# Kernel tuning notes

Hardware: AMD Instinct MI355X
Metric: run time of the kernel (lower is better)

## Reference

```python
import jax, jax.numpy as jnp
import numpy as np

N_NODES = 50000
N_EDGES = 600000
BAG = 16
VOCAB = 10000
EMB = 128
HID = 128
N_CLASSES = 10
N_GRAPHS = 512
PAD_IDX = 1


def setup_inputs() -> dict:
    key = jax.random.key(0)
    ks = jax.random.split(key, 12)
    x_tokens = jax.random.randint(ks[0], (N_NODES, BAG), 0, VOCAB)
    src = jax.random.randint(ks[1], (N_EDGES,), 0, N_NODES)
    dst = jax.random.randint(ks[2], (N_EDGES,), 0, N_NODES)
    edge_index = jnp.stack([src, dst])
    batch = jnp.sort(jax.random.randint(ks[3], (N_NODES,), 0, N_GRAPHS))
    # rows 0,1 are zero in the original (weights[2:] filled from pretrained vectors)
    emb_table = (jax.random.normal(ks[4], (VOCAB, EMB)) * 0.02).at[:2].set(0.0)
    s = 1.0 / np.sqrt(EMB)
    w1_l = jax.random.normal(ks[5], (HID, EMB)) * s
    b1 = jnp.zeros((HID,), jnp.float32)
    w1_r = jax.random.normal(ks[6], (HID, EMB)) * s
    w2_l = jax.random.normal(ks[7], (HID, HID)) * s
    b2 = jnp.zeros((HID,), jnp.float32)
    w2_r = jax.random.normal(ks[8], (HID, HID)) * s
    w_out = jax.random.normal(ks[9], (N_CLASSES, HID)) * s
    b_out = jnp.zeros((N_CLASSES,), jnp.float32)
    return {"x_tokens": x_tokens, "edge_index": edge_index, "batch": batch,
            "emb_table": emb_table, "w1_l": w1_l, "b1": b1, "w1_r": w1_r,
            "w2_l": w2_l, "b2": b2, "w2_r": w2_r, "w_out": w_out, "b_out": b_out}


def _embedding_bag_mean(tokens, table):
    # nn.EmbeddingBag mode='mean' with padding_idx: padding tokens excluded from mean
    emb = table[tokens]                                  # [N, BAG, D]
    mask = (tokens != PAD_IDX)[..., None].astype(table.dtype)
    total = jnp.sum(emb * mask, axis=1)                  # [N, D]
    cnt = jnp.clip(jnp.sum(mask, axis=1), 1.0)           # [N, 1]
    return total / cnt


def _sage_conv(x, src, dst, w_l, b_l, w_r):
    # PyG SAGEConv: lin_l(mean_{j in N(i)} x_j) + lin_r(x_i); lin_r has no bias
    n = x.shape[0]
    msg_sum = jax.ops.segment_sum(x[src], dst, num_segments=n)           # [N, D]
    deg = jax.ops.segment_sum(jnp.ones((src.shape[0], 1), x.dtype), dst,
                              num_segments=n)                             # [N, 1]
    aggr = msg_sum / jnp.clip(deg, 1.0)
    return aggr @ w_l.T + b_l + x @ w_r.T


def reference(x_tokens, edge_index, batch, emb_table, w1_l, b1, w1_r,
              w2_l, b2, w2_r, w_out, b_out):
    src, dst = edge_index[0], edge_index[1]
    x = _embedding_bag_mean(x_tokens, emb_table)                 # [N, EMB]
    x = jax.nn.relu(_sage_conv(x, src, dst, w1_l, b1, w1_r))     # [N, HID]
    x = jax.nn.relu(_sage_conv(x, src, dst, w2_l, b2, w2_r))     # [N, HID]
    # global_mean_pool over graph ids
    g_sum = jax.ops.segment_sum(x, batch, num_segments=N_GRAPHS)
    g_cnt = jax.ops.segment_sum(jnp.ones((x.shape[0], 1), x.dtype), batch,
                                num_segments=N_GRAPHS)
    g = g_sum / jnp.clip(g_cnt, 1.0)                             # [G, HID]
    return g @ w_out.T + b_out                                   # [G, C]
```

## Files before the change

### kernel.cpp

```cpp
#include <hip/hip_runtime.h>
#include <hip/hip_bf16.h>

#define NN 50000
#define NE 600000
#define BAG 16
#define EMB 128
#define HID 128
#define NC 10
#define NG 512
#define PAD_IDX 1
#define VOCAB 10000
#define SLOTS 64
#define TPAIRS (VOCAB * EMB / 2)
#define WPAIRS (4 * HID * EMB / 2)
#define EMVB (NN / 16)
#define NTILES ((NN + 127) / 128)

typedef __attribute__((ext_vector_type(8))) short v8s;
typedef __attribute__((ext_vector_type(4))) float v4f;

__device__ __forceinline__ float bflo(unsigned u) { return __uint_as_float(u << 16); }
__device__ __forceinline__ float bfhi(unsigned u) { return __uint_as_float(u & 0xffff0000u); }
__device__ __forceinline__ unsigned short f2bf(float f) {
    unsigned u = __float_as_uint(f);
    return (unsigned short)((u + 0x7fffu + ((u >> 16) & 1u)) >> 16);
}
__device__ __forceinline__ void acc8(float* a, v8s v) {
    unsigned* u = (unsigned*)&v;
#pragma unroll
    for (int j = 0; j < 4; j++) {
        a[2 * j] += bflo(u[j]);
        a[2 * j + 1] += bfhi(u[j]);
    }
}

__global__ void k_conv(const float* __restrict__ t, unsigned short* __restrict__ tb,
                       const float* __restrict__ w1l, const float* __restrict__ w1r,
                       const float* __restrict__ w2l, const float* __restrict__ w2r,
                       unsigned short* __restrict__ wbf, int* __restrict__ cnt,
                       float* __restrict__ gsum, float* __restrict__ gcnt) {
    int i = blockIdx.x * blockDim.x + threadIdx.x;
    if (i < NN) cnt[i] = 0;
    if (i < NG * HID) gsum[i] = 0.f;
    if (i < NG) gcnt[i] = 0.f;
    if (i < TPAIRS) {
        float2 v = *(const float2*)(t + (size_t)i * 2);
        unsigned lo = f2bf(v.x), hi = f2bf(v.y);
        *(unsigned*)(tb + (size_t)i * 2) = lo | (hi << 16);
    } else if (i < TPAIRS + WPAIRS) {
        int j = i - TPAIRS;
        int k = j * 2;
        int arr = k >> 14;
        int o = k & 16383;
        const float* w = (arr == 0) ? w1l : (arr == 1) ? w1r : (arr == 2) ? w2l : w2r;
        float2 v = *(const float2*)(w + o);
        unsigned lo = f2bf(v.x), hi = f2bf(v.y);
        *(unsigned*)(wbf + k) = lo | (hi << 16);
    }
}

__global__ __launch_bounds__(256) void k_scatem(const int* __restrict__ src,
                                                const int* __restrict__ dst,
                                                int* __restrict__ cnt,
                                                int* __restrict__ slots,
                                                const int* __restrict__ tokens,
                                                const unsigned short* __restrict__ table,
                                                unsigned short* __restrict__ x0) {
    int b = blockIdx.x;
    int tid = threadIdx.x;

    int e = b * 256 + tid;
    int s_src = 0, s_dst = 0, p = SLOTS;
    bool has_e = (e < NE);
    if (has_e) {
        s_src = src[e];
        s_dst = dst[e];
        p = atomicAdd(&cnt[s_dst], 1);
    }

    int sl = tid & 15;
    int node = b * 16 + (tid >> 4);
    const int* tp = tokens + node * BAG;
    int tk[16];
    *(int4*)(tk) = *(const int4*)(tp);
    *(int4*)(tk + 4) = *(const int4*)(tp + 4);
    *(int4*)(tk + 8) = *(const int4*)(tp + 8);
    *(int4*)(tk + 12) = *(const int4*)(tp + 12);
    int c = 0;
#pragma unroll
    for (int t = 0; t < BAG; t++) c += (tk[t] != PAD_IDX);
    float a[8];
#pragma unroll
    for (int j = 0; j < 8; j++) a[j] = 0.f;
#pragma unroll
    for (int h = 0; h < 2; h++) {
        v8s v[8];
#pragma unroll
        for (int t = 0; t < 8; t++)
            v[t] = *(const v8s*)(table + (size_t)tk[h * 8 + t] * EMB + sl * 8);
#pragma unroll
        for (int t = 0; t < 8; t++) acc8(a, v[t]);
    }
    float inv = 1.0f / (float)(c > 0 ? c : 1);
    uint4 o;
    o.x = f2bf(a[0] * inv) | ((unsigned)f2bf(a[1] * inv) << 16);
    o.y = f2bf(a[2] * inv) | ((unsigned)f2bf(a[3] * inv) << 16);
    o.z = f2bf(a[4] * inv) | ((unsigned)f2bf(a[5] * inv) << 16);
    o.w = f2bf(a[6] * inv) | ((unsigned)f2bf(a[7] * inv) << 16);
    *(uint4*)(x0 + (size_t)node * EMB + sl * 8) = o;

    if (has_e && p < SLOTS) slots[(size_t)s_dst * SLOTS + p] = s_src;
}

__global__ __launch_bounds__(256) void k_aggr(const unsigned short* __restrict__ x,
                                              const int* __restrict__ cnt,
                                              const int* __restrict__ slots,
                                              unsigned short* __restrict__ aggr) {
    int node = blockIdx.x * 4 + (threadIdx.x >> 6);
    int lane = threadIdx.x & 63;
    if (node >= NN) return;
    int deg = cnt[node];
    int m = deg > SLOTS ? SLOTS : deg;
    int g = lane >> 4, sl = lane & 15;
    float a[8];
#pragma unroll
    for (int j = 0; j < 8; j++) a[j] = 0.f;
    int idx_l = slots[(size_t)node * SLOTS + ((lane < m) ? lane : 0)];
    int i = 0;
    for (; i + 8 <= m; i += 8) {
        int t0 = __shfl(idx_l, i + g, 64);
        int t1 = __shfl(idx_l, i + 4 + g, 64);
        v8s v0 = *(const v8s*)(x + (size_t)t0 * HID + sl * 8);
        v8s v1 = *(const v8s*)(x + (size_t)t1 * HID + sl * 8);
        acc8(a, v0);
        acc8(a, v1);
    }
    for (; i + 4 <= m; i += 4) {
        int t0 = __shfl(idx_l, i + g, 64);
        v8s v0 = *(const v8s*)(x + (size_t)t0 * HID + sl * 8);
        acc8(a, v0);
    }
    int rem = m - i;
    if (rem > 0) {
        int t0 = __shfl(idx_l, (g < rem) ? i + g : i, 64);
        v8s v0 = *(const v8s*)(x + (size_t)t0 * HID + sl * 8);
        if (g < rem) acc8(a, v0);
    }
#pragma unroll
    for (int j = 0; j < 8; j++) {
        a[j] += __shfl_xor(a[j], 16, 64);
        a[j] += __shfl_xor(a[j], 32, 64);
    }
    float inv = 1.0f / (float)(deg > 0 ? deg : 1);
    if (g == 0) {
        uint4 o;
        o.x = f2bf(a[0] * inv) | ((unsigned)f2bf(a[1] * inv) << 16);
        o.y = f2bf(a[2] * inv) | ((unsigned)f2bf(a[3] * inv) << 16);
        o.z = f2bf(a[4] * inv) | ((unsigned)f2bf(a[5] * inv) << 16);
        o.w = f2bf(a[6] * inv) | ((unsigned)f2bf(a[7] * inv) << 16);
        *(uint4*)(aggr + (size_t)node * HID + sl * 8) = o;
    }
}

__device__ __forceinline__ void sage_kloop(int row0, const unsigned short* __restrict__ xa,
                                           const unsigned short* __restrict__ xr,
                                           const unsigned short* __restrict__ wl,
                                           const unsigned short* __restrict__ wr,
                                           unsigned short* As, unsigned short* Bs,
                                           v4f acc[2][8]) {
    int tid = threadIdx.x;
    int wave = tid >> 6, lane = tid & 63;
    int q = lane >> 4, l16 = lane & 15;
    for (int kc = 0; kc < 8; kc++) {
        const unsigned short* Ag = (kc < 4) ? xa : xr;
        const unsigned short* Bg = (kc < 4) ? wl : wr;
        int koff = (kc & 3) * 32;
#pragma unroll
        for (int it = 0; it < 2; it++) {
            int seg = tid + it * 256;
            int r = seg >> 2, sg = seg & 3;
            int gr = row0 + r;
            if (gr > NN - 1) gr = NN - 1;
            v8s a = *(const v8s*)(Ag + (size_t)gr * HID + koff + sg * 8);
            *(v8s*)(As + r * 32 + sg * 8) = a;
            v8s b = *(const v8s*)(Bg + (size_t)r * HID + koff + sg * 8);
            *(v8s*)(Bs + r * 32 + sg * 8) = b;
        }
        __syncthreads();
        v8s a0 = *(const v8s*)(As + (wave * 32 + l16) * 32 + q * 8);
        v8s a1 = *(const v8s*)(As + (wave * 32 + 16 + l16) * 32 + q * 8);
#pragma unroll
        for (int nt = 0; nt < 8; nt++) {
            v8s b = *(const v8s*)(Bs + (nt * 16 + l16) * 32 + q * 8);
            acc[0][nt] = __builtin_amdgcn_mfma_f32_16x16x32_bf16(a0, b, acc[0][nt], 0, 0, 0);
            acc[1][nt] = __builtin_amdgcn_mfma_f32_16x16x32_bf16(a1, b, acc[1][nt], 0, 0, 0);
        }
        __syncthreads();
    }
}

__global__ __launch_bounds__(256) void k_sage(const unsigned short* __restrict__ xa,
                                              const unsigned short* __restrict__ xr,
                                              const unsigned short* __restrict__ wl,
                                              const unsigned short* __restrict__ wr,
                                              const float* __restrict__ bias,
                                              unsigned short* __restrict__ out) {
    __shared__ unsigned short As[128 * 32];
    __shared__ unsigned short Bs[128 * 32];
    int row0 = blockIdx.x * 128;
    v4f acc[2][8];
#pragma unroll
    for (int m = 0; m < 2; m++)
#pragma unroll
        for (int n = 0; n < 8; n++) acc[m][n] = (v4f){0.f, 0.f, 0.f, 0.f};
    sage_kloop(row0, xa, xr, wl, wr, As, Bs, acc);
    int tid = threadIdx.x;
    int wave = tid >> 6, lane = tid & 63;
    int q = lane >> 4, l16 = lane & 15;
#pragma unroll
    for (int nt = 0; nt < 8; nt++) {
        int col = nt * 16 + l16;
        float bv = bias[col];
#pragma unroll
        for (int mt = 0; mt < 2; mt++) {
#pragma unroll
            for (int r = 0; r < 4; r++) {
                int row = row0 + wave * 32 + mt * 16 + q * 4 + r;
                if (row < NN) {
                    float v = acc[mt][nt][r] + bv;
                    v = v > 0.f ? v : 0.f;
                    out[(size_t)row * HID + col] = f2bf(v);
                }
            }
        }
    }
}

__global__ __launch_bounds__(256) void k_sagepool(const unsigned short* __restrict__ xa,
                                                  const unsigned short* __restrict__ xr,
                                                  const unsigned short* __restrict__ wl,
                                                  const unsigned short* __restrict__ wr,
                                                  const float* __restrict__ bias,
                                                  const int* __restrict__ batch,
                                                  float* __restrict__ gsum,
                                                  float* __restrict__ gcnt) {
    __shared__ unsigned short smem[128 * 128];
    unsigned short* As = smem;
    unsigned short* Bs = smem + 128 * 32;
    int row0 = blockIdx.x * 128;
    v4f acc[2][8];
#pragma unroll
    for (int m = 0; m < 2; m++)
#pragma unroll
        for (int n = 0; n < 8; n++) acc[m][n] = (v4f){0.f, 0.f, 0.f, 0.f};
    sage_kloop(row0, xa, xr, wl, wr, As, Bs, acc);
    int tid = threadIdx.x;
    int wave = tid >> 6, lane = tid & 63;
    int q = lane >> 4, l16 = lane & 15;
#pragma unroll
    for (int nt = 0; nt < 8; nt++) {
        int col = nt * 16 + l16;
        float bv = bias[col];
#pragma unroll
        for (int mt = 0; mt < 2; mt++) {
#pragma unroll
            for (int r = 0; r < 4; r++) {
                int rl = wave * 32 + mt * 16 + q * 4 + r;
                float v = acc[mt][nt][r] + bv;
                v = v > 0.f ? v : 0.f;
                smem[rl * 128 + col] = f2bf(v);
            }
        }
    }
    __syncthreads();
    if (tid < 128) {
        int col = tid;
        int end = NN - row0;
        if (end > 128) end = 128;
        int cur = batch[row0];
        float acc_p = 0.f;
        int c = 0;
        for (int i = 0; i < end; i++) {
            int b = batch[row0 + i];
            if (b != cur) {
                atomicAdd(&gsum[cur * HID + col], acc_p);
                if (col == 0) atomicAdd(&gcnt[cur], (float)c);
                acc_p = 0.f;
                c = 0;
                cur = b;
            }
            acc_p += __uint_as_float(((unsigned)smem[i * 128 + col]) << 16);
            c++;
        }
        atomicAdd(&gsum[cur * HID + col], acc_p);
        if (col == 0) atomicAdd(&gcnt[cur], (float)c);
    }
}

__global__ __launch_bounds__(128) void k_final(const float* __restrict__ gsum,
                                               const float* __restrict__ gcnt,
                                               const float* __restrict__ w_out,
                                               const float* __restrict__ b_out,
                                               float* __restrict__ out) {
    __shared__ float mean[HID];
    int g = blockIdx.x, tid = threadIdx.x;
    mean[tid] = gsum[g * HID + tid] / fmaxf(gcnt[g], 1.0f);
    __syncthreads();
    if (tid < NC) {
        float s = b_out[tid];
#pragma unroll 16
        for (int d = 0; d < HID; d++) s += mean[d] * w_out[tid * HID + d];
        out[g * NC + tid] = s;
    }
}

extern "C" void kernel_launch(void* const* d_in, const int* in_sizes, int n_in,
                              void* d_out, int out_size, void* d_ws, size_t ws_size,
                              hipStream_t stream) {
    const int* x_tokens = (const int*)d_in[0];
    const int* edge = (const int*)d_in[1];
    const int* batch = (const int*)d_in[2];
    const float* emb_table = (const float*)d_in[3];
    const float* w1l = (const float*)d_in[4];
    const float* b1 = (const float*)d_in[5];
    const float* w1r = (const float*)d_in[6];
    const float* w2l = (const float*)d_in[7];
    const float* b2 = (const float*)d_in[8];
    const float* w2r = (const float*)d_in[9];
    const float* w_out = (const float*)d_in[10];
    const float* b_out = (const float*)d_in[11];
    float* out = (float*)d_out;

    char* ws = (char*)d_ws;
    size_t off = 0;
    auto alloc = [&](size_t bytes) {
        void* p = ws + off;
        off += (bytes + 255) & ~(size_t)255;
        return p;
    };
    int* cnt = (int*)alloc(NN * 4);
    int* slots = (int*)alloc((size_t)NN * SLOTS * 4);
    unsigned short* wbf = (unsigned short*)alloc(4 * HID * EMB * 2);
    float* gsum = (float*)alloc(NG * HID * 4);
    float* gcnt = (float*)alloc(NG * 4);
    unsigned short* x0 = (unsigned short*)alloc((size_t)NN * EMB * 2);
    unsigned short* x1 = (unsigned short*)alloc((size_t)NN * HID * 2);
    unsigned short* aggrb = (unsigned short*)alloc((size_t)NN * HID * 2);
    unsigned short* table_bf = x1;

    const int* srcp = edge;
    const int* dstp = edge + NE;

    k_conv<<<(TPAIRS + WPAIRS + 255) / 256, 256, 0, stream>>>(
        emb_table, table_bf, w1l, w1r, w2l, w2r, wbf, cnt, gsum, gcnt);
    k_scatem<<<EMVB, 256, 0, stream>>>(srcp, dstp, cnt, slots, x_tokens,
                                       table_bf, x0);
    k_aggr<<<(NN + 3) / 4, 256, 0, stream>>>(x0, cnt, slots, aggrb);
    k_sage<<<NTILES, 256, 0, stream>>>(aggrb, x0, wbf, wbf + 16384, b1, x1);
    k_aggr<<<(NN + 3) / 4, 256, 0, stream>>>(x1, cnt, slots, aggrb);
    k_sagepool<<<NTILES, 256, 0, stream>>>(aggrb, x1, wbf + 32768, wbf + 49152, b2,
                                           batch, gsum, gcnt);
    k_final<<<NG, 128, 0, stream>>>(gsum, gcnt, w_out, b_out, out);
}
```

Baseline: 205.9 us.

## Partition edge scatter by destination range and store neighbor slots as 16-bit

Result: no change. 208.9 us (+1.5%).

```diff
diff --git a/kernel.cpp b/kernel.cpp
--- a/kernel.cpp
+++ b/kernel.cpp
@@ -14,6 +14,9 @@
 #define TPAIRS (VOCAB * EMB / 2)
 #define WPAIRS (4 * HID * EMB / 2)
 #define EMVB (NN / 16)
+#define NCHUNK 293
+#define SCB (NCHUNK * 8)
+#define NRANGE (NN / 8)
 #define NTILES ((NN + 127) / 128)
 
 typedef __attribute__((ext_vector_type(8))) short v8s;
@@ -62,24 +65,38 @@
 __global__ __launch_bounds__(256) void k_scatem(const int* __restrict__ src,
                                                 const int* __restrict__ dst,
                                                 int* __restrict__ cnt,
-                                                int* __restrict__ slots,
+                                                unsigned short* __restrict__ slots,
                                                 const int* __restrict__ tokens,
                                                 const unsigned short* __restrict__ table,
                                                 unsigned short* __restrict__ x0) {
     int b = blockIdx.x;
     int tid = threadIdx.x;
 
-    int e = b * 256 + tid;
-    int s_src = 0, s_dst = 0, p = SLOTS;
-    bool has_e = (e < NE);
-    if (has_e) {
-        s_src = src[e];
-        s_dst = dst[e];
-        p = atomicAdd(&cnt[s_dst], 1);
+    if (b < SCB) {
+        int r = b & 7, c = b >> 3;
+        int e0 = c * 2048 + tid * 8;
+        if (e0 < NE) {
+            int lo = r * NRANGE, hi = lo + NRANGE;
+            int4 s0 = *((const int4*)(src + e0));
+            int4 s1 = *((const int4*)(src + e0) + 1);
+            int4 d0 = *((const int4*)(dst + e0));
+            int4 d1 = *((const int4*)(dst + e0) + 1);
+            int ss[8] = {s0.x, s0.y, s0.z, s0.w, s1.x, s1.y, s1.z, s1.w};
+            int dd[8] = {d0.x, d0.y, d0.z, d0.w, d1.x, d1.y, d1.z, d1.w};
+#pragma unroll
+            for (int j = 0; j < 8; j++) {
+                if (dd[j] >= lo && dd[j] < hi) {
+                    int p = atomicAdd(&cnt[dd[j]], 1);
+                    if (p < SLOTS)
+                        slots[(size_t)dd[j] * SLOTS + p] = (unsigned short)ss[j];
+                }
+            }
+        }
+        return;
     }
 
     int sl = tid & 15;
-    int node = b * 16 + (tid >> 4);
+    int node = (b - SCB) * 16 + (tid >> 4);
     const int* tp = tokens + node * BAG;
     int tk[16];
     *(int4*)(tk) = *(const int4*)(tp);
@@ -108,13 +125,11 @@
     o.z = f2bf(a[4] * inv) | ((unsigned)f2bf(a[5] * inv) << 16);
     o.w = f2bf(a[6] * inv) | ((unsigned)f2bf(a[7] * inv) << 16);
     *(uint4*)(x0 + (size_t)node * EMB + sl * 8) = o;
-
-    if (has_e && p < SLOTS) slots[(size_t)s_dst * SLOTS + p] = s_src;
 }
 
 __global__ __launch_bounds__(256) void k_aggr(const unsigned short* __restrict__ x,
                                               const int* __restrict__ cnt,
-                                              const int* __restrict__ slots,
+                                              const unsigned short* __restrict__ slots,
                                               unsigned short* __restrict__ aggr) {
     int node = blockIdx.x * 4 + (threadIdx.x >> 6);
     int lane = threadIdx.x & 63;
@@ -339,7 +354,7 @@
         return p;
     };
     int* cnt = (int*)alloc(NN * 4);
-    int* slots = (int*)alloc((size_t)NN * SLOTS * 4);
+    unsigned short* slots = (unsigned short*)alloc((size_t)NN * SLOTS * 2);
     unsigned short* wbf = (unsigned short*)alloc(4 * HID * EMB * 2);
     float* gsum = (float*)alloc(NG * HID * 4);
     float* gcnt = (float*)alloc(NG * 4);
@@ -353,8 +368,8 @@
 
     k_conv<<<(TPAIRS + WPAIRS + 255) / 256, 256, 0, stream>>>(
         emb_table, table_bf, w1l, w1r, w2l, w2r, wbf, cnt, gsum, gcnt);
-    k_scatem<<<EMVB, 256, 0, stream>>>(srcp, dstp, cnt, slots, x_tokens,
-                                       table_bf, x0);
+    k_scatem<<<SCB + EMVB, 256, 0, stream>>>(srcp, dstp, cnt, slots, x_tokens,
+                                             table_bf, x0);
     k_aggr<<<(NN + 3) / 4, 256, 0, stream>>>(x0, cnt, slots, aggrb);
     k_sage<<<NTILES, 256, 0, stream>>>(aggrb, x0, wbf, wbf + 16384, b1, x1);
     k_aggr<<<(NN + 3) / 4, 256, 0, stream>>>(x1, cnt, slots, aggrb);
```
